# Kernel tuning notes

Measured on AMD Instinct MI355X. Metric: run time of the kernel, lower is better.

## Reference

```python
import jax, jax.numpy as jnp
import numpy as np

IMG = 32            # feature-map side == image_size
B, HC = 8, 3        # batch, hint channels
C, NH, L = 256, 8, 8  # model_channels, nhead, num_encoder_layers
DFF = 1025
HIN = IMG * 8       # hint resolution (three stride-2 convs => /8)
NEIGH = (7, 7)
CONV_SHAPES = [(16, HC), (16, 16), (32, 16), (32, 32), (96, 32), (96, 96), (256, 96), (C, 256)]
STRIDES = [1, 1, 2, 1, 2, 1, 2, 1]


def setup_inputs() -> dict:
    key = jax.random.key(0)
    ks = jax.random.split(key, 32)
    inp = {"hint": jax.random.normal(ks[0], (B, HC, HIN, HIN), jnp.float32)}
    for i, (co, ci) in enumerate(CONV_SHAPES):
        inp[f"conv_w{i}"] = jax.random.normal(ks[1 + i], (co, ci, 3, 3), jnp.float32) * 0.05
    base = 9
    def p(shape, j):
        return jax.random.normal(ks[base + j], (L,) + shape, jnp.float32) * 0.02
    inp["in_proj_w"] = p((3 * C, C), 0)
    inp["in_proj_b"] = p((3 * C,), 1)
    inp["out_w"] = p((C, C), 2)
    inp["out_b"] = p((C,), 3)
    inp["lin1_w"] = p((DFF, C), 4)
    inp["lin1_b"] = p((DFF,), 5)
    inp["lin2_w"] = p((C, DFF), 6)
    inp["lin2_b"] = p((C,), 7)
    inp["ln1_w"] = jnp.ones((L, C), jnp.float32)
    inp["ln1_b"] = jnp.zeros((L, C), jnp.float32)
    inp["ln2_w"] = jnp.ones((L, C), jnp.float32)
    inp["ln2_b"] = jnp.zeros((L, C), jnp.float32)
    return inp


def _conv(x, w, s):
    # torch Conv2d(k=3, padding=1, stride=s, bias=False)
    return jax.lax.conv_general_dilated(x, w, (s, s), [(1, 1), (1, 1)],
                                        dimension_numbers=("NCHW", "OIHW", "NCHW"))


def _sine_pos(h, w, c):
    # DETR/UniAD PositionEmbeddingSine (normalize=False, temperature=1e4) -> (h*w, c)
    npf = c // 2
    y = jnp.broadcast_to(jnp.arange(1, h + 1, dtype=jnp.float32)[:, None], (h, w))
    x = jnp.broadcast_to(jnp.arange(1, w + 1, dtype=jnp.float32)[None, :], (h, w))
    dim_t = 10000.0 ** (2.0 * (jnp.arange(npf, dtype=jnp.float32) // 2) / npf)
    px = x[..., None] / dim_t
    py = y[..., None] / dim_t
    px = jnp.stack([jnp.sin(px[..., 0::2]), jnp.cos(px[..., 1::2])], -1).reshape(h, w, npf)
    py = jnp.stack([jnp.sin(py[..., 0::2]), jnp.cos(py[..., 1::2])], -1).reshape(h, w, npf)
    return jnp.concatenate([py, px], -1).reshape(h * w, c)


def _neigh_mask(h, w, hm, wm):
    # vectorized version of generate_mask: 0 inside the hm x wm neighborhood, -inf outside
    ih = jnp.arange(h)
    iw = jnp.arange(w)
    dh = jnp.abs(ih[:, None] - ih[None, :]) <= hm // 2   # (h, h)
    dw = jnp.abs(iw[:, None] - iw[None, :]) <= wm // 2   # (w, w)
    allowed = (dh[:, None, :, None] & dw[None, :, None, :]).reshape(h * w, h * w)
    return jnp.where(allowed, 0.0, -1e9).astype(jnp.float32)


def _ln(x, g, b):
    mu = x.mean(-1, keepdims=True)
    v = ((x - mu) ** 2).mean(-1, keepdims=True)
    return (x - mu) / jnp.sqrt(v + 1e-5) * g + b


def _forward(hint, conv_ws, params):
    x = hint
    for i, (w, s) in enumerate(zip(conv_ws, STRIDES)):
        x = _conv(x, w, s)
        if i < len(conv_ws) - 1:
            x = jax.nn.silu(x)
    b, c, h, w = x.shape
    src = x.reshape(b, c, h * w).transpose(0, 2, 1)          # (B, N, C), N h-major
    pos = _sine_pos(h, w, c)[None]                           # (1, N, C)
    mask = _neigh_mask(h, w, *NEIGH)                         # (N, N)
    dh = c // NH
    scale = 1.0 / np.sqrt(dh).astype(np.float32)

    def layer(s, p):
        ipw, ipb, ow, ob, l1w, l1b, l2w, l2b, g1, b1, g2, b2 = p
        qk_in = s + pos
        q = (qk_in @ ipw[:c].T + ipb[:c]).reshape(b, -1, NH, dh)
        k = (qk_in @ ipw[c:2 * c].T + ipb[c:2 * c]).reshape(b, -1, NH, dh)
        v = (s @ ipw[2 * c:].T + ipb[2 * c:]).reshape(b, -1, NH, dh)
        sc = jnp.einsum('bnhd,bmhd->bhnm', q, k) * scale + mask
        a = jax.nn.softmax(sc, -1)
        ctx = jnp.einsum('bhnm,bmhd->bnhd', a, v).reshape(b, -1, c)
        s = _ln(s + ctx @ ow.T + ob, g1, b1)                 # post-norm
        ff = jax.nn.relu(s @ l1w.T + l1b) @ l2w.T + l2b      # dropout inactive (eval)
        return _ln(s + ff, g2, b2), None

    src, _ = jax.lax.scan(layer, src, params)
    return src.transpose(0, 2, 1).reshape(b, c, h, w)        # '(h w) b c -> b c h w'


def reference(hint, conv_w0, conv_w1, conv_w2, conv_w3, conv_w4, conv_w5, conv_w6, conv_w7,
              in_proj_w, in_proj_b, out_w, out_b, lin1_w, lin1_b, lin2_w, lin2_b,
              ln1_w, ln1_b, ln2_w, ln2_b):
    conv_ws = (conv_w0, conv_w1, conv_w2, conv_w3, conv_w4, conv_w5, conv_w6, conv_w7)
    params = (in_proj_w, in_proj_b, out_w, out_b, lin1_w, lin1_b, lin2_w, lin2_b,
              ln1_w, ln1_b, ln2_w, ln2_b)
    return _forward(hint, conv_ws, params)
```

## Files before the change

kernel.cpp:

```cpp
#include <hip/hip_runtime.h>
#include <hip/hip_bf16.h>


typedef __bf16 bf16x8 __attribute__((ext_vector_type(8)));
typedef float f32x4 __attribute__((ext_vector_type(4)));
typedef unsigned short us8v __attribute__((ext_vector_type(8)));

__device__ __forceinline__ unsigned short f2bf(float f) {
  unsigned int u = __float_as_uint(f);
  unsigned int r = (u + 0x7fffu + ((u >> 16) & 1u)) >> 16;
  return (unsigned short)r;
}
__device__ __forceinline__ float bf2f(unsigned short h) {
  return __uint_as_float(((unsigned int)h) << 16);
}

#define GLD16(src, dst)                                                        \
  __builtin_amdgcn_global_load_lds(                                            \
      (const __attribute__((address_space(1))) unsigned int*)(src),            \
      (__attribute__((address_space(3))) unsigned int*)(dst), 16, 0, 0)

template<int BM, int BN, int NT, int MODE, int LNF = 0, int KTC = 0>
__global__ __launch_bounds__(NT) void k_gemm(
    const unsigned short* __restrict__ A, int lda,
    const unsigned short* __restrict__ Bw, int ldb,
    const float* __restrict__ bias, const float* __restrict__ posadd,
    float* __restrict__ C, unsigned short* __restrict__ Cb, int ldc,
    int K, int Nstore, int act, int omode, long long zsB, long long zsC,
    const unsigned short* __restrict__ zpage, int Ci, int Hi, int stride, int lw,
    int divm, int divs, const float* __restrict__ lng, const float* __restrict__ lnb)
{
  constexpr int NW = NT / 64;
  constexpr int NWN = (NT == 512) ? 4 : ((BN >= 128) ? 2 : 1);
  constexpr int NWM = NW / NWN;
  constexpr int WM = BM / NWM, WN = BN / NWN;
  constexpr int MF = WM / 16, NF = WN / 16;
  constexpr int AIS = (BM * 8) / NT;
  constexpr int BIS = (BN * 8) / NT;
  __shared__ unsigned short lA[2][BM * 64];
  __shared__ unsigned short lB[2][BN * 64];
  __shared__ float red[2][32][2];
  int tid = threadIdx.x, lane = tid & 63, wid = tid >> 6;
  int bm = blockIdx.x * BM, bn = blockIdx.y * BN;
  const unsigned short* Bz = Bw + (size_t)blockIdx.z * zsB;

  int j = (lane & 7) ^ (lane >> 3);
  int e8 = (j & 3) << 3;
  int halfl = j >> 2;

  size_t arow[AIS], brow[BIS];
  int hb[AIS], wb[AIS];
  size_t ab[AIS];
#pragma unroll
  for (int i = 0; i < AIS; ++i) {
    int rr = (wid + i * NW) * 8 + (lane >> 3);
    if constexpr (MODE == 0) {
      arow[i] = (size_t)(bm + rr) * lda + (j << 3);
    } else {
      int pos = bm + rr;
      int b = pos >> (2 * lw);
      int rem = pos & ((1 << (2 * lw)) - 1);
      int ho = rem >> lw, wo = rem & ((1 << lw) - 1);
      hb[i] = ho * stride - 1;
      wb[i] = wo * stride - 1;
      ab[i] = (size_t)b * Hi * Hi * Ci;
    }
  }
#pragma unroll
  for (int i = 0; i < BIS; ++i)
    brow[i] = (size_t)(bn + (wid + i * NW) * 8 + (lane >> 3)) * ldb + (j << 3);

  auto stage = [&](int buf, int kt) {
    if constexpr (MODE == 1) {
      int s0 = kt * 2, s1 = s0 + 1;
      int t0 = (s0 * divm) >> divs, t1 = (s1 * divm) >> divs;
      int cipw = Ci >> 5;
      int cc0 = (s0 - t0 * cipw) << 5, cc1 = (s1 - t1 * cipw) << 5;
      int kh0 = (t0 * 171) >> 9, kw0 = t0 - kh0 * 3;
      int kh1 = (t1 * 171) >> 9, kw1 = t1 - kh1 * 3;
      int kh = halfl ? kh1 : kh0;
      int kw = halfl ? kw1 : kw0;
      int cco = halfl ? cc1 : cc0;
      bool tv = (halfl ? t1 : t0) < 9;
#pragma unroll
      for (int i = 0; i < AIS; ++i) {
        int hi = hb[i] + kh, wi = wb[i] + kw;
        const unsigned short* ap =
            (tv && (unsigned)hi < (unsigned)Hi && (unsigned)wi < (unsigned)Hi)
                ? (A + ab[i] + (size_t)(hi * Hi + wi) * Ci + cco + e8)
                : zpage;
        GLD16(ap, &lA[buf][(wid + i * NW) * 512]);
      }
    } else {
#pragma unroll
      for (int i = 0; i < AIS; ++i)
        GLD16(A + arow[i] + kt * 64, &lA[buf][(wid + i * NW) * 512]);
    }
#pragma unroll
    for (int i = 0; i < BIS; ++i)
      GLD16(Bz + brow[i] + kt * 64, &lB[buf][(wid + i * NW) * 512]);
  };

  f32x4 acc[MF][NF];
#pragma unroll
  for (int m = 0; m < MF; ++m)
#pragma unroll
    for (int n = 0; n < NF; ++n)
#pragma unroll
      for (int q = 0; q < 4; ++q) acc[m][n][q] = 0.f;

  int wn = wid % NWN, wm = wid / NWN;
  int r0 = wm * WM + (lane & 15);
  int c0 = wn * WN + (lane & 15);
  int sl0 = (((lane >> 4)) ^ (lane & 7)) << 3;
  int sl1 = (((lane >> 4) + 4) ^ (lane & 7)) << 3;
  const int nkt = (KTC > 0) ? KTC : (K >> 6);
  int cur = 0;
  stage(0, 0);
#pragma unroll
  for (int kt = 0; kt < nkt; ++kt) {
    if (kt + 1 < nkt) {
      stage(cur ^ 1, kt + 1);
      asm volatile("s_waitcnt vmcnt(%0)" : : "n"(AIS + BIS) : "memory");
    } else {
      asm volatile("s_waitcnt vmcnt(0)" : : : "memory");
    }
    __builtin_amdgcn_s_barrier();
    asm volatile("" ::: "memory");
    bf16x8 a0[MF], a1[MF], b0[NF], b1[NF];
#pragma unroll
    for (int m = 0; m < MF; ++m) {
      a0[m] = *(const bf16x8*)&lA[cur][(r0 + m * 16) * 64 + sl0];
      a1[m] = *(const bf16x8*)&lA[cur][(r0 + m * 16) * 64 + sl1];
    }
#pragma unroll
    for (int n = 0; n < NF; ++n) {
      b0[n] = *(const bf16x8*)&lB[cur][(c0 + n * 16) * 64 + sl0];
      b1[n] = *(const bf16x8*)&lB[cur][(c0 + n * 16) * 64 + sl1];
    }
#pragma unroll
    for (int m = 0; m < MF; ++m)
#pragma unroll
      for (int n = 0; n < NF; ++n)
        acc[m][n] = __builtin_amdgcn_mfma_f32_16x16x32_bf16(a0[m], b0[n], acc[m][n], 0, 0, 0);
#pragma unroll
    for (int m = 0; m < MF; ++m)
#pragma unroll
      for (int n = 0; n < NF; ++n)
        acc[m][n] = __builtin_amdgcn_mfma_f32_16x16x32_bf16(a1[m], b1[n], acc[m][n], 0, 0, 0);
    asm volatile("" ::: "memory");
    __builtin_amdgcn_s_barrier();
    cur ^= 1;
  }

  int colb = bn + wn * WN + (lane & 15);
  int rowb = bm + wm * WM + ((lane >> 4) << 2);

  if constexpr (LNF) {
    float x[NF][4];
    float sums[4] = {0.f, 0.f, 0.f, 0.f}, sqs[4] = {0.f, 0.f, 0.f, 0.f};
#pragma unroll
    for (int n = 0; n < NF; ++n) {
      int col = colb + n * 16;
      float bs = bias[col];
#pragma unroll
      for (int q = 0; q < 4; ++q) {
        int row = rowb + q;
        float v = acc[0][n][q] + bs + C[(size_t)row * 256 + col];
        x[n][q] = v;
        sums[q] += v;
        sqs[q] += v * v;
      }
    }
#pragma unroll
    for (int q = 0; q < 4; ++q) {
      sums[q] += __shfl_xor(sums[q], 1); sqs[q] += __shfl_xor(sqs[q], 1);
      sums[q] += __shfl_xor(sums[q], 2); sqs[q] += __shfl_xor(sqs[q], 2);
      sums[q] += __shfl_xor(sums[q], 4); sqs[q] += __shfl_xor(sqs[q], 4);
      sums[q] += __shfl_xor(sums[q], 8); sqs[q] += __shfl_xor(sqs[q], 8);
    }
    int rl = wm * 16 + ((lane >> 4) << 2);
    if ((lane & 15) == 0) {
#pragma unroll
      for (int q = 0; q < 4; ++q) {
        red[wn][rl + q][0] = sums[q];
        red[wn][rl + q][1] = sqs[q];
      }
    }
    __syncthreads();
#pragma unroll
    for (int q = 0; q < 4; ++q) {
      float ts = sums[q] + red[wn ^ 1][rl + q][0];
      float tq = sqs[q] + red[wn ^ 1][rl + q][1];
      float mu = ts * (1.f / 256.f);
      float var = tq * (1.f / 256.f) - mu * mu;
      float rs = rsqrtf(var + 1e-5f);
      int row = rowb + q;
#pragma unroll
      for (int n = 0; n < NF; ++n) {
        int col = colb + n * 16;
        float o = (x[n][q] - mu) * rs * lng[col] + lnb[col];
        C[(size_t)row * 256 + col] = o;
        Cb[(size_t)row * 256 + col] = f2bf(o);
      }
    }
    return;
  }

  float* Cz = C ? C + (size_t)blockIdx.z * zsC : nullptr;
  unsigned short* Cbz = Cb ? Cb + (size_t)blockIdx.z * zsC : nullptr;
#pragma unroll
  for (int n = 0; n < NF; ++n) {
    int col = colb + n * 16;
    if (col >= Nstore) continue;
    float bs = bias ? bias[col] : 0.f;
#pragma unroll
    for (int m = 0; m < MF; ++m) {
#pragma unroll
      for (int q = 0; q < 4; ++q) {
        int row = rowb + m * 16 + q;
        float v = acc[m][n][q] + bs;
        if (posadd && col < 512) v += posadd[((row & 1023) << 9) + col];
        if (act == 1) v = fmaxf(v, 0.f);
        else if (act == 2) v = v / (1.f + __expf(-v));
        size_t off = (size_t)row * ldc + col;
        if (omode == 0) Cz[off] = v;
        else if (omode == 1) Cbz[off] = f2bf(v);
        else { Cz[off] = v; Cbz[off] = f2bf(v); }
      }
    }
  }
}

__global__ __launch_bounds__(256) void k_conv0(
    const float* __restrict__ x, const float* __restrict__ w,
    unsigned short* __restrict__ y)
{
  __shared__ float ws[16][28];
  int tid = threadIdx.x;
  for (int u = tid; u < 432; u += 256) {
    int co = u / 27, k = u - co * 27;
    int t = k / 3, ci = k - t * 3;
    ws[co][k] = w[((size_t)co * 3 + ci) * 9 + t];
  }
  __syncthreads();
  int h = blockIdx.x, b = blockIdx.y, wo = tid;
  float xin[3][3][3];
#pragma unroll
  for (int ci = 0; ci < 3; ++ci)
#pragma unroll
    for (int kh = 0; kh < 3; ++kh) {
      int hi = h + kh - 1;
#pragma unroll
      for (int kw = 0; kw < 3; ++kw) {
        int wi = wo + kw - 1;
        xin[ci][kh][kw] = ((unsigned)hi < 256u && (unsigned)wi < 256u)
            ? x[(((size_t)b * 3 + ci) << 16) + (hi << 8) + wi] : 0.f;
      }
    }
  float acc[16] = {};
#pragma unroll
  for (int t = 0; t < 9; ++t) {
    const int kh = t / 3, kw = t % 3;
#pragma unroll
    for (int ci = 0; ci < 3; ++ci) {
      float xv = xin[ci][kh][kw];
#pragma unroll
      for (int co = 0; co < 16; ++co)
        acc[co] = fmaf(xv, ws[co][t * 3 + ci], acc[co]);
    }
  }
  us8v o0, o1, zv;
#pragma unroll
  for (int q = 0; q < 8; ++q) {
    float v0 = acc[q];     v0 = v0 / (1.f + __expf(-v0)); o0[q] = f2bf(v0);
    float v1 = acc[q + 8]; v1 = v1 / (1.f + __expf(-v1)); o1[q] = f2bf(v1);
    zv[q] = 0;
  }
  unsigned short* yp = y + ((((size_t)b << 16) + (h << 8) + wo) << 5);
  *(us8v*)(yp) = o0; *(us8v*)(yp + 8) = o1;
  *(us8v*)(yp + 16) = zv; *(us8v*)(yp + 24) = zv;
}

template<int S>
__global__ __launch_bounds__(256) void k_conv_direct(
    const unsigned short* __restrict__ x, const unsigned short* __restrict__ wp,
    int ldw, unsigned short* __restrict__ y, int Hi, int Ho, int Wo, int lwt)
{
  constexpr int HR = 7 * S + 3;
  constexpr int HC = 15 * S + 3;
  constexpr int HP = HR * HC;
  __shared__ unsigned short xs[HP * 40];
  __shared__ unsigned short wsh[32 * 312];
  int tid = threadIdx.x, lane = tid & 63, wv = tid >> 6;
  int b = blockIdx.y;
  int tr = blockIdx.x >> lwt, tc = blockIdx.x & ((1 << lwt) - 1);
  int hi0 = tr * 8 * S - 1, wi0 = tc * 16 * S - 1;

  for (int u = tid; u < HP * 8; u += 256) {
    int pix = u >> 3, part = u & 7;
    int hr = pix / HC, hcc = pix - hr * HC;
    int hi = hi0 + hr, wi = wi0 + hcc;
    ushort4 v = {0, 0, 0, 0};
    if ((unsigned)hi < (unsigned)Hi && (unsigned)wi < (unsigned)Hi)
      v = *(const ushort4*)(x + ((size_t)(b * Hi + hi) * Hi + wi) * 32 + part * 4);
    *(ushort4*)(&xs[pix * 40 + part * 4]) = v;
  }
  for (int u = tid; u < 2304; u += 256) {
    int co = u / 72, kk = (u - co * 72) * 4;
    *(ushort4*)(&wsh[co * 312 + kk]) = *(const ushort4*)(wp + (size_t)co * ldw + kk);
  }
  __syncthreads();

  int cL = lane & 15, kq = (lane >> 4) << 3;
  f32x4 acc[2][2];
#pragma unroll
  for (int m = 0; m < 2; ++m)
#pragma unroll
    for (int n = 0; n < 2; ++n)
#pragma unroll
      for (int q = 0; q < 4; ++q) acc[m][n][q] = 0.f;

#pragma unroll
  for (int tap = 0; tap < 9; ++tap) {
    const int kh = tap / 3, kw = tap % 3;
    bf16x8 af[2], bfr[2];
#pragma unroll
    for (int m = 0; m < 2; ++m) {
      int hr = (wv * 2 + m) * S + kh;
      int hc = cL * S + kw;
      af[m] = *(const bf16x8*)&xs[(hr * HC + hc) * 40 + kq];
    }
#pragma unroll
    for (int n = 0; n < 2; ++n)
      bfr[n] = *(const bf16x8*)&wsh[(cL + n * 16) * 312 + tap * 32 + kq];
#pragma unroll
    for (int m = 0; m < 2; ++m)
#pragma unroll
      for (int n = 0; n < 2; ++n)
        acc[m][n] = __builtin_amdgcn_mfma_f32_16x16x32_bf16(af[m], bfr[n], acc[m][n], 0, 0, 0);
  }

  int wo0 = tc * 16 + ((lane >> 4) << 2);
#pragma unroll
  for (int m = 0; m < 2; ++m) {
    int ho = tr * 8 + wv * 2 + m;
#pragma unroll
    for (int n = 0; n < 2; ++n) {
      int co = cL + n * 16;
#pragma unroll
      for (int q = 0; q < 4; ++q) {
        float v = acc[m][n][q];
        v = v / (1.f + __expf(-v));
        y[((size_t)(b * Ho + ho) * Wo + wo0 + q) * 32 + co] = f2bf(v);
      }
    }
  }
}

struct WP8 { const float* w[8]; unsigned short* q[8]; };
__global__ __launch_bounds__(256) void k_wperm_all(WP8 p)
{
  const int CoPs[8]  = {128, 32, 32, 32, 128, 128, 256, 256};
  const int CiRs[8]  = {3, 16, 16, 32, 32, 96, 96, 256};
  const int CiPs[8]  = {3, 32, 32, 32, 32, 96, 96, 256};
  const int Kpads[8] = {64, 288, 288, 288, 320, 896, 896, 2304};
  const int Cos[8]   = {16, 16, 32, 32, 96, 96, 256, 256};
  int i = blockIdx.y + 1;
  const float* w = p.w[i];
  unsigned short* wp = p.q[i];
  int Kpad = Kpads[i], CiP = CiPs[i], CiR = CiRs[i], Co = Cos[i];
  int total = CoPs[i] * Kpad;
  for (int idx = blockIdx.x * 256 + threadIdx.x; idx < total; idx += gridDim.x * 256) {
    int co = idx / Kpad, k = idx - co * Kpad;
    int t = k / CiP, ci = k - t * CiP;
    float v = 0.f;
    if (co < Co && t < 9 && ci < CiR) v = w[((size_t)co * CiR + ci) * 9 + t];
    wp[idx] = f2bf(v);
  }
}

__global__ void k_cvt_pad(const float* __restrict__ in, unsigned short* __restrict__ outb,
                          float* __restrict__ outf, int R, int C, int Rp, int Cp)
{
  int l = blockIdx.y;
  int total = Rp * Cp;
  for (int idx = blockIdx.x * 256 + threadIdx.x; idx < total; idx += gridDim.x * 256) {
    int r = idx / Cp, c = idx - r * Cp;
    float v = (r < R && c < C) ? in[((size_t)l * R + r) * C + c] : 0.f;
    size_t o = (size_t)l * total + idx;
    if (outb) outb[o] = f2bf(v);
    if (outf) outf[o] = v;
  }
}

__global__ __launch_bounds__(256) void k_pos(unsigned short* __restrict__ posb)
{
  int n = blockIdx.x, c = threadIdx.x;
  int ih = n >> 5, iw = n & 31;
  float coord = (c < 128) ? (float)(ih + 1) : (float)(iw + 1);
  int cc = c & 127;
  float e = (float)((cc >> 1) << 1) * (1.f / 128.f);
  float t = coord / powf(10000.f, e);
  posb[(n << 8) + c] = f2bf((cc & 1) ? cosf(t) : sinf(t));
}

__global__ __launch_bounds__(256) void k_attn(
    const unsigned short* __restrict__ qkv, unsigned short* __restrict__ ctx)
{
  __shared__ unsigned short k_ldsu[848 * 8];
  __shared__ unsigned short v_lds[848 * 8];
  __shared__ float p_lds[64 * 50];
  int bx = blockIdx.x;
  int b = bx >> 4, tile = bx & 15;
  int th8 = ((tile >> 2) << 3), tw8 = ((tile & 3) << 3);
  int g = blockIdx.y;
  int tid = threadIdx.x, lane = tid & 63, wid = tid >> 6;
  int h0e = max(th8 - 3, 0), h1e = min(th8 + 10, 31);
  int w0e = max(tw8 - 3, 0), w1e = min(tw8 + 10, 31);
  int nh = h1e - h0e + 1, nw = w1e - w0e + 1;
  int nkeys = nh * nw, nslots = nkeys * 4;
  unsigned int magic = (65536u + (unsigned)nw - 1u) / (unsigned)nw;
  size_t qbase = (size_t)((unsigned)b << 10) * 768;

#pragma unroll
  for (int i = 0; i < 4; ++i) {
    int base = i * 256 + wid * 64;
    if (base < 784) {
      int s = min(base + lane, nslots - 1);
      int uidx = s >> 2, chunk = s & 3;
      int hh = (int)(((unsigned)uidx * magic) >> 16);
      int ww = uidx - hh * nw;
      hh += h0e; ww += w0e;
      const unsigned short* rp = qkv + qbase + (size_t)((hh << 5) + ww) * 768 + (g << 5) + chunk * 8;
      GLD16(rp + 256, &k_ldsu[base * 8]);
      GLD16(rp + 512, &v_lds[base * 8]);
    }
  }
  __syncthreads();

  int q = tid >> 2, dq = tid & 3;
  int qh = th8 + (q >> 3), qw = tw8 + (q & 7);
  const float scale = 0.17677669529663687f;
  const unsigned short* qp = qkv + qbase + (size_t)((qh << 5) + qw) * 768 + (g << 5) + dq * 8;
  us8v uq = *(const us8v*)qp;
  float qr[8];
#pragma unroll
  for (int t = 0; t < 8; ++t) qr[t] = bf2f(uq[t]) * scale;

  int rbase[7], cofs[7];
  bool rval[7], cval[7];
#pragma unroll
  for (int d = 0; d < 7; ++d) {
    int mh = qh - 3 + d;
    rval[d] = (unsigned)mh < 32u;
    rbase[d] = (mh - h0e) * nw;
    int mw = qw - 3 + d;
    cval[d] = (unsigned)mw < 32u;
    cofs[d] = mw - w0e;
  }

  float m = -1e30f;
#pragma unroll
  for (int kk = 0; kk < 49; ++kk) {
    const int d7 = kk / 7, r7 = kk % 7;
    bool valid = rval[d7] && cval[r7];
    int uidx = valid ? (rbase[d7] + cofs[r7]) : 0;
    us8v uk = *(const us8v*)&k_ldsu[uidx * 32 + dq * 8];
    float d = 0.f;
#pragma unroll
    for (int t = 0; t < 8; ++t) d = fmaf(qr[t], bf2f(uk[t]), d);
    d += __shfl_xor(d, 1);
    d += __shfl_xor(d, 2);
    float s_kk = valid ? d : -1e30f;
    m = fmaxf(m, s_kk);
    if (dq == (kk & 3)) p_lds[q * 50 + kk] = s_kk;
  }
  float sum = 0.f;
  for (int kk = dq; kk < 49; kk += 4) {
    float e = __expf(p_lds[q * 50 + kk] - m);
    p_lds[q * 50 + kk] = e;
    sum += e;
  }
  sum += __shfl_xor(sum, 1);
  sum += __shfl_xor(sum, 2);
  float inv = 1.f / sum;

  float acc[8] = {};
#pragma unroll
  for (int kk = 0; kk < 49; ++kk) {
    const int d7 = kk / 7, r7 = kk % 7;
    int uidx = (rval[d7] && cval[r7]) ? (rbase[d7] + cofs[r7]) : 0;
    float pb = p_lds[q * 50 + kk];
    us8v uv = *(const us8v*)&v_lds[uidx * 32 + dq * 8];
#pragma unroll
    for (int t = 0; t < 8; ++t) acc[t] = fmaf(pb, bf2f(uv[t]), acc[t]);
  }
  unsigned short* op = ctx + ((size_t)((b << 10) + (qh << 5) + qw) << 8) + (g << 5) + dq * 8;
  us8v out;
#pragma unroll
  for (int t = 0; t < 8; ++t) out[t] = f2bf(acc[t] * inv);
  *(us8v*)op = out;
}

__global__ void k_nxc_to_cxn(const float* __restrict__ x, float* __restrict__ y)
{
  __shared__ float t[32][33];
  int b = blockIdx.z;
  int c0 = blockIdx.x * 32, n0 = blockIdx.y * 32;
  int tx = threadIdx.x, ty = threadIdx.y;
  t[ty][tx] = x[((size_t)(b * 1024 + n0 + ty)) * 256 + c0 + tx];
  __syncthreads();
  y[((size_t)(b * 256 + c0 + ty)) * 1024 + n0 + tx] = t[tx][ty];
}

extern "C" void kernel_launch(void* const* d_in, const int* in_sizes, int n_in,
                              void* d_out, int out_size, void* d_ws, size_t ws_size,
                              hipStream_t stream)
{
  const float* hint = (const float*)d_in[0];
  const float* cw[8];
  for (int i = 0; i < 8; ++i) cw[i] = (const float*)d_in[1 + i];
  const float* ipw  = (const float*)d_in[9];
  const float* ipb  = (const float*)d_in[10];
  const float* outw = (const float*)d_in[11];
  const float* outb = (const float*)d_in[12];
  const float* l1w  = (const float*)d_in[13];
  const float* l1b  = (const float*)d_in[14];
  const float* l2w  = (const float*)d_in[15];
  const float* l2b  = (const float*)d_in[16];
  const float* g1   = (const float*)d_in[17];
  const float* b1   = (const float*)d_in[18];
  const float* g2   = (const float*)d_in[19];
  const float* b2   = (const float*)d_in[20];

  float* ws = (float*)d_ws;
  size_t off = 0;
  float* bufA = ws + off; off += 8388608;
  float* bufB = ws + off; off += 8388608;
  float* src  = ws + off; off += 2097152;
  unsigned short* srcb = (unsigned short*)(ws + off); off += 1048576;
  unsigned short* posb = (unsigned short*)(ws + off); off += 131072;
  float* posqk = ws + off; off += 4194304;
  unsigned short* wqkvb = (unsigned short*)(ws + off); off += 786432;
  unsigned short* outwb = (unsigned short*)(ws + off); off += 262144;
  unsigned short* l1wb  = (unsigned short*)(ws + off); off += 1179648;
  unsigned short* l2wb  = (unsigned short*)(ws + off); off += 1179648;
  float* l1bp = ws + off; off += 9216;
  unsigned short* cwp[8];
  const int CoPs[8]  = {128, 32, 32, 32, 128, 128, 256, 256};
  const int Kpads[8] = {64, 288, 288, 288, 320, 896, 896, 2304};
  for (int i = 0; i < 8; ++i) { cwp[i] = (unsigned short*)(ws + off); off += ((size_t)CoPs[i] * Kpads[i] + 1) / 2; }
  unsigned short* zpage = (unsigned short*)(ws + off); off += 64;

  hipMemsetAsync(zpage, 0, 256, stream);

  k_cvt_pad<<<dim3(768, 8), 256, 0, stream>>>(ipw,  wqkvb, nullptr, 768, 256, 768, 256);
  k_cvt_pad<<<dim3(256, 8), 256, 0, stream>>>(outw, outwb, nullptr, 256, 256, 256, 256);
  k_cvt_pad<<<dim3(1152, 8), 256, 0, stream>>>(l1w, l1wb, nullptr, 1025, 256, 1152, 256);
  k_cvt_pad<<<dim3(1152, 8), 256, 0, stream>>>(l2w, l2wb, nullptr, 256, 1025, 256, 1152);
  k_cvt_pad<<<dim3(5, 8), 256, 0, stream>>>(l1b, nullptr, l1bp, 1025, 1, 1152, 1);
  WP8 wpargs;
  for (int i = 0; i < 8; ++i) { wpargs.w[i] = cw[i]; wpargs.q[i] = cwp[i]; }
  k_wperm_all<<<dim3(64, 7), 256, 0, stream>>>(wpargs);
  k_pos<<<dim3(1024), 256, 0, stream>>>(posb);

  unsigned short* bufAu = (unsigned short*)bufA;
  unsigned short* bufBu = (unsigned short*)bufB;

#define GEMM_TAIL nullptr, 0, 0, 0, 0, 0, 0, nullptr, nullptr
  k_conv0<<<dim3(256, 8), 256, 0, stream>>>(hint, cw[0], bufAu);
  k_conv_direct<1><<<dim3(512, 8), 256, 0, stream>>>(bufAu, cwp[1], 288, bufBu, 256, 256, 256, 4);
  k_conv_direct<2><<<dim3(128, 8), 256, 0, stream>>>(bufBu, cwp[2], 288, bufAu, 256, 128, 128, 3);
  k_conv_direct<1><<<dim3(128, 8), 256, 0, stream>>>(bufAu, cwp[3], 288, bufBu, 128, 128, 128, 3);
  k_gemm<128, 128, 512, 1, 0, 5><<<dim3(256, 1), 512, 0, stream>>>(
      bufBu, 0, cwp[4], 320, nullptr, nullptr, nullptr, bufAu, 96, 320, 96, 2, 1,
      0, 0, zpage, 32, 128, 2, 6, 1, 0, nullptr, nullptr);
  k_gemm<128, 128, 512, 1, 0, 14><<<dim3(256, 1), 512, 0, stream>>>(
      bufAu, 0, cwp[5], 896, nullptr, nullptr, nullptr, bufBu, 96, 896, 96, 2, 1,
      0, 0, zpage, 96, 64, 1, 6, 171, 9, nullptr, nullptr);
  k_gemm<64, 128, 512, 1, 0, 14><<<dim3(128, 2), 512, 0, stream>>>(
      bufBu, 0, cwp[6], 896, nullptr, nullptr, nullptr, bufAu, 256, 896, 256, 2, 1,
      0, 0, zpage, 96, 64, 2, 5, 171, 9, nullptr, nullptr);
  k_gemm<64, 128, 512, 1><<<dim3(128, 2), 512, 0, stream>>>(
      bufAu, 0, cwp[7], 2304, nullptr, nullptr, src, srcb, 256, 2304, 256, 0, 2,
      0, 0, zpage, 256, 32, 1, 5, 1, 3, nullptr, nullptr);

  k_gemm<64, 128, 512, 0, 0, 4><<<dim3(16, 4, 8), 512, 0, stream>>>(
      posb, 256, wqkvb, 256, nullptr, nullptr, posqk, nullptr, 512, 256, 512, 0, 0,
      196608LL, 524288LL, GEMM_TAIL);

  unsigned short* qkvb = bufAu;
  unsigned short* ctx  = (unsigned short*)(bufA + 3145728);
  unsigned short* ff   = (unsigned short*)(bufB + 2097152);

  for (int l = 0; l < 8; ++l) {
    const unsigned short* wqkv_l = wqkvb + (size_t)l * 768 * 256;
    const float* ipb_l  = ipb  + (size_t)l * 768;
    const unsigned short* outw_l = outwb + (size_t)l * 256 * 256;
    const float* outb_l = outb + (size_t)l * 256;
    const unsigned short* l1w_l = l1wb + (size_t)l * 1152 * 256;
    const float* l1b_l  = l1bp + (size_t)l * 1152;
    const unsigned short* l2w_l = l2wb + (size_t)l * 256 * 1152;
    const float* l2b_l  = l2b  + (size_t)l * 256;
    const float* posqk_l = posqk + (size_t)l * 524288;
    const float* g1_l = g1 + l * 256; const float* b1_l = b1 + l * 256;
    const float* g2_l = g2 + l * 256; const float* b2_l = b2 + l * 256;

    k_gemm<64, 128, 512, 0, 0, 4><<<dim3(128, 6), 512, 0, stream>>>(
        srcb, 256, wqkv_l, 256, ipb_l, posqk_l, nullptr, qkvb, 768, 256, 768, 0, 1,
        0, 0, GEMM_TAIL);
    k_attn<<<dim3(128, 8), 256, 0, stream>>>(qkvb, ctx);
    k_gemm<32, 256, 256, 0, 1, 4><<<dim3(256, 1), 256, 0, stream>>>(
        ctx, 256, outw_l, 256, outb_l, nullptr, src, srcb, 256, 256, 256, 0, 0,
        0, 0, nullptr, 0, 0, 0, 0, 0, 0, g1_l, b1_l);
    k_gemm<64, 128, 512, 0, 0, 4><<<dim3(128, 9), 512, 0, stream>>>(
        srcb, 256, l1w_l, 256, l1b_l, nullptr, nullptr, ff, 1152, 256, 1152, 1, 1,
        0, 0, GEMM_TAIL);
    k_gemm<32, 256, 256, 0, 1, 18><<<dim3(256, 1), 256, 0, stream>>>(
        ff, 1152, l2w_l, 1152, l2b_l, nullptr, src, srcb, 256, 1152, 256, 0, 0,
        0, 0, nullptr, 0, 0, 0, 0, 0, 0, g2_l, b2_l);
  }

  k_nxc_to_cxn<<<dim3(8, 32, 8), dim3(32, 32), 0, stream>>>(src, (float*)d_out);
}
```

Baseline: 911.9 us.

## Fuse FFN lin1+ReLU+lin2+LayerNorm into one kernel; merge prep launches

Adds a fused FFN kernel in which each 32-row block computes the lin1 GEMM with bias and ReLU into a 32x1152 bf16 LDS tile, then runs the lin2 GEMM, residual add and LayerNorm without writing the intermediate to global memory. It uses double-buffered global-to-LDS weight staging. This removes one launch per layer and the global round-trip of the 8192x1152 intermediate. The trade-off is 256 blocks with very large LDS use (about 140KB), so occupancy is low and the weights are re-read by every block. Separately, the weight-conversion and positional-embedding setup kernels are merged into one launch.

```diff
diff --git a/kernel.cpp b/kernel.cpp
--- a/kernel.cpp
+++ b/kernel.cpp
@@ -232,6 +232,191 @@
   }
 }
 
+__global__ __launch_bounds__(256) void k_ffn(
+    const unsigned short* __restrict__ srcb, const unsigned short* __restrict__ w1,
+    const float* __restrict__ b1, const unsigned short* __restrict__ w2,
+    const float* __restrict__ b2, float* __restrict__ src,
+    unsigned short* __restrict__ sbo,
+    const float* __restrict__ lng, const float* __restrict__ lnb)
+{
+  __shared__ unsigned short aT[4][32 * 64];
+  __shared__ unsigned short lB[2][256 * 64];
+  __shared__ unsigned short ffl[32][1160];
+  __shared__ float red[2][32][2];
+  int tid = threadIdx.x, lane = tid & 63, wid = tid >> 6;
+  int bm = blockIdx.x << 5;
+  int j = (lane & 7) ^ (lane >> 3);
+  int rsrc = (lane >> 3);
+
+  {
+    int rr = wid * 8 + rsrc;
+    const unsigned short* ap = srcb + (size_t)(bm + rr) * 256 + (j << 3);
+#pragma unroll
+    for (int kt = 0; kt < 4; ++kt)
+      GLD16(ap + kt * 64, &aT[kt][wid * 512]);
+  }
+  size_t brow1[4], brow2[8];
+#pragma unroll
+  for (int i = 0; i < 4; ++i)
+    brow1[i] = (size_t)((wid + i * 4) * 8 + rsrc) * 256 + (j << 3);
+#pragma unroll
+  for (int i = 0; i < 8; ++i)
+    brow2[i] = (size_t)((wid + i * 4) * 8 + rsrc) * 1152 + (j << 3);
+
+  auto stageB1 = [&](int buf, int s) {
+    int ny = s >> 2, kt = s & 3;
+#pragma unroll
+    for (int i = 0; i < 4; ++i)
+      GLD16(w1 + (size_t)ny * 128 * 256 + brow1[i] + kt * 64, &lB[buf][(wid + i * 4) * 512]);
+  };
+  auto stageB2 = [&](int buf, int kt) {
+#pragma unroll
+    for (int i = 0; i < 8; ++i)
+      GLD16(w2 + brow2[i] + kt * 64, &lB[buf][(wid + i * 4) * 512]);
+  };
+
+  int wn = wid & 1, wm = wid >> 1;
+  int r0 = wm * 16 + (lane & 15);
+  int sl0 = (((lane >> 4)) ^ (lane & 7)) << 3;
+  int sl1 = (((lane >> 4) + 4) ^ (lane & 7)) << 3;
+  int kqa = (lane >> 4) << 3;
+
+  stageB1(0, 0);
+  int cur = 0;
+  for (int ny = 0; ny < 9; ++ny) {
+    f32x4 acc1[4];
+#pragma unroll
+    for (int n = 0; n < 4; ++n)
+#pragma unroll
+      for (int q = 0; q < 4; ++q) acc1[n][q] = 0.f;
+    int c01 = wn * 64 + (lane & 15);
+#pragma unroll
+    for (int kt = 0; kt < 4; ++kt) {
+      int s = ny * 4 + kt;
+      if (s + 1 < 36) {
+        stageB1(cur ^ 1, s + 1);
+        asm volatile("s_waitcnt vmcnt(4)" : : : "memory");
+      } else {
+        asm volatile("s_waitcnt vmcnt(0)" : : : "memory");
+      }
+      __builtin_amdgcn_s_barrier();
+      asm volatile("" ::: "memory");
+      bf16x8 a0 = *(const bf16x8*)&aT[kt][r0 * 64 + sl0];
+      bf16x8 a1 = *(const bf16x8*)&aT[kt][r0 * 64 + sl1];
+      bf16x8 b0v[4], b1v[4];
+#pragma unroll
+      for (int n = 0; n < 4; ++n) {
+        b0v[n] = *(const bf16x8*)&lB[cur][(c01 + n * 16) * 64 + sl0];
+        b1v[n] = *(const bf16x8*)&lB[cur][(c01 + n * 16) * 64 + sl1];
+      }
+#pragma unroll
+      for (int n = 0; n < 4; ++n)
+        acc1[n] = __builtin_amdgcn_mfma_f32_16x16x32_bf16(a0, b0v[n], acc1[n], 0, 0, 0);
+#pragma unroll
+      for (int n = 0; n < 4; ++n)
+        acc1[n] = __builtin_amdgcn_mfma_f32_16x16x32_bf16(a1, b1v[n], acc1[n], 0, 0, 0);
+      asm volatile("" ::: "memory");
+      __builtin_amdgcn_s_barrier();
+      cur ^= 1;
+    }
+    int rowl = wm * 16 + ((lane >> 4) << 2);
+#pragma unroll
+    for (int n = 0; n < 4; ++n) {
+      int col = ny * 128 + c01 + n * 16;
+      float bs = b1[col];
+#pragma unroll
+      for (int q = 0; q < 4; ++q)
+        ffl[rowl + q][col] = f2bf(fmaxf(acc1[n][q] + bs, 0.f));
+    }
+  }
+
+  stageB2(0, 0);
+  __syncthreads();
+  cur = 0;
+  f32x4 acc[8];
+#pragma unroll
+  for (int n = 0; n < 8; ++n)
+#pragma unroll
+    for (int q = 0; q < 4; ++q) acc[n][q] = 0.f;
+  int c02 = wn * 128 + (lane & 15);
+#pragma unroll
+  for (int kt = 0; kt < 18; ++kt) {
+    if (kt + 1 < 18) {
+      stageB2(cur ^ 1, kt + 1);
+      asm volatile("s_waitcnt vmcnt(8)" : : : "memory");
+    } else {
+      asm volatile("s_waitcnt vmcnt(0)" : : : "memory");
+    }
+    __builtin_amdgcn_s_barrier();
+    asm volatile("" ::: "memory");
+    bf16x8 a0 = *(const bf16x8*)&ffl[r0][kt * 64 + kqa];
+    bf16x8 a1 = *(const bf16x8*)&ffl[r0][kt * 64 + 32 + kqa];
+    bf16x8 b0v[8], b1v[8];
+#pragma unroll
+    for (int n = 0; n < 8; ++n) {
+      b0v[n] = *(const bf16x8*)&lB[cur][(c02 + n * 16) * 64 + sl0];
+      b1v[n] = *(const bf16x8*)&lB[cur][(c02 + n * 16) * 64 + sl1];
+    }
+#pragma unroll
+    for (int n = 0; n < 8; ++n)
+      acc[n] = __builtin_amdgcn_mfma_f32_16x16x32_bf16(a0, b0v[n], acc[n], 0, 0, 0);
+#pragma unroll
+    for (int n = 0; n < 8; ++n)
+      acc[n] = __builtin_amdgcn_mfma_f32_16x16x32_bf16(a1, b1v[n], acc[n], 0, 0, 0);
+    asm volatile("" ::: "memory");
+    __builtin_amdgcn_s_barrier();
+    cur ^= 1;
+  }
+
+  int rowl = wm * 16 + ((lane >> 4) << 2);
+  float x[8][4];
+  float sums[4] = {0.f, 0.f, 0.f, 0.f}, sqs[4] = {0.f, 0.f, 0.f, 0.f};
+#pragma unroll
+  for (int n = 0; n < 8; ++n) {
+    int col = c02 + n * 16;
+    float bs = b2[col];
+#pragma unroll
+    for (int q = 0; q < 4; ++q) {
+      int row = bm + rowl + q;
+      float v = acc[n][q] + bs + src[(size_t)row * 256 + col];
+      x[n][q] = v;
+      sums[q] += v;
+      sqs[q] += v * v;
+    }
+  }
+#pragma unroll
+  for (int q = 0; q < 4; ++q) {
+    sums[q] += __shfl_xor(sums[q], 1); sqs[q] += __shfl_xor(sqs[q], 1);
+    sums[q] += __shfl_xor(sums[q], 2); sqs[q] += __shfl_xor(sqs[q], 2);
+    sums[q] += __shfl_xor(sums[q], 4); sqs[q] += __shfl_xor(sqs[q], 4);
+    sums[q] += __shfl_xor(sums[q], 8); sqs[q] += __shfl_xor(sqs[q], 8);
+  }
+  if ((lane & 15) == 0) {
+#pragma unroll
+    for (int q = 0; q < 4; ++q) {
+      red[wn][rowl + q][0] = sums[q];
+      red[wn][rowl + q][1] = sqs[q];
+    }
+  }
+  __syncthreads();
+#pragma unroll
+  for (int q = 0; q < 4; ++q) {
+    float ts = sums[q] + red[wn ^ 1][rowl + q][0];
+    float tq = sqs[q] + red[wn ^ 1][rowl + q][1];
+    float mu = ts * (1.f / 256.f);
+    float var = tq * (1.f / 256.f) - mu * mu;
+    float rs = rsqrtf(var + 1e-5f);
+    int row = bm + rowl + q;
+#pragma unroll
+    for (int n = 0; n < 8; ++n) {
+      int col = c02 + n * 16;
+      float o = (x[n][q] - mu) * rs * lng[col] + lnb[col];
+      src[(size_t)row * 256 + col] = o;
+      sbo[(size_t)row * 256 + col] = f2bf(o);
+    }
+  }
+}
+
 __global__ __launch_bounds__(256) void k_conv0(
     const float* __restrict__ x, const float* __restrict__ w,
     unsigned short* __restrict__ y)
@@ -380,29 +565,48 @@
   }
 }
 
-__global__ void k_cvt_pad(const float* __restrict__ in, unsigned short* __restrict__ outb,
-                          float* __restrict__ outf, int R, int C, int Rp, int Cp)
+struct PrepArgs {
+  const float *ipw, *outw, *l1w, *l2w, *l1b;
+  unsigned short *wqkvb, *outwb, *l1wb, *l2wb, *posb;
+  float *l1bp;
+};
+__global__ __launch_bounds__(256) void k_prep(PrepArgs a)
 {
-  int l = blockIdx.y;
-  int total = Rp * Cp;
-  for (int idx = blockIdx.x * 256 + threadIdx.x; idx < total; idx += gridDim.x * 256) {
-    int r = idx / Cp, c = idx - r * Cp;
-    float v = (r < R && c < C) ? in[((size_t)l * R + r) * C + c] : 0.f;
-    size_t o = (size_t)l * total + idx;
-    if (outb) outb[o] = f2bf(v);
-    if (outf) outf[o] = v;
-  }
-}
-
-__global__ __launch_bounds__(256) void k_pos(unsigned short* __restrict__ posb)
-{
-  int n = blockIdx.x, c = threadIdx.x;
-  int ih = n >> 5, iw = n & 31;
-  float coord = (c < 128) ? (float)(ih + 1) : (float)(iw + 1);
-  int cc = c & 127;
-  float e = (float)((cc >> 1) << 1) * (1.f / 128.f);
-  float t = coord / powf(10000.f, e);
-  posb[(n << 8) + c] = f2bf((cc & 1) ? cosf(t) : sinf(t));
+  int seg = blockIdx.y;
+  int idx0 = blockIdx.x * 256 + threadIdx.x;
+  int stride = gridDim.x * 256;
+  if (seg == 0) {
+    for (int i = idx0; i < 8 * 768 * 256; i += stride) a.wqkvb[i] = f2bf(a.ipw[i]);
+  } else if (seg == 1) {
+    for (int i = idx0; i < 8 * 256 * 256; i += stride) a.outwb[i] = f2bf(a.outw[i]);
+  } else if (seg == 2) {
+    for (int i = idx0; i < 8 * 1152 * 256; i += stride) {
+      int l = i / (1152 * 256), r = (i >> 8) % 1152, c = i & 255;
+      float v = (r < 1025) ? a.l1w[((size_t)l * 1025 + r) * 256 + c] : 0.f;
+      a.l1wb[i] = f2bf(v);
+    }
+  } else if (seg == 3) {
+    for (int i = idx0; i < 8 * 256 * 1152; i += stride) {
+      int l = i / (256 * 1152), rc = i % (256 * 1152), r = rc / 1152, c = rc - (rc / 1152) * 1152;
+      float v = (c < 1025) ? a.l2w[((size_t)l * 256 + r) * 1025 + c] : 0.f;
+      a.l2wb[i] = f2bf(v);
+    }
+  } else if (seg == 4) {
+    for (int i = idx0; i < 8 * 1152; i += stride) {
+      int l = i / 1152, c = i - l * 1152;
+      a.l1bp[i] = (c < 1025) ? a.l1b[l * 1025 + c] : 0.f;
+    }
+  } else {
+    for (int i = idx0; i < 1024 * 256; i += stride) {
+      int n = i >> 8, c = i & 255;
+      int ih = n >> 5, iw = n & 31;
+      float coord = (c < 128) ? (float)(ih + 1) : (float)(iw + 1);
+      int cc = c & 127;
+      float e = (float)((cc >> 1) << 1) * (1.f / 128.f);
+      float t = coord / powf(10000.f, e);
+      a.posb[i] = f2bf((cc & 1) ? cosf(t) : sinf(t));
+    }
+  }
 }
 
 __global__ __launch_bounds__(256) void k_attn(
@@ -555,15 +759,14 @@
 
   hipMemsetAsync(zpage, 0, 256, stream);
 
-  k_cvt_pad<<<dim3(768, 8), 256, 0, stream>>>(ipw,  wqkvb, nullptr, 768, 256, 768, 256);
-  k_cvt_pad<<<dim3(256, 8), 256, 0, stream>>>(outw, outwb, nullptr, 256, 256, 256, 256);
-  k_cvt_pad<<<dim3(1152, 8), 256, 0, stream>>>(l1w, l1wb, nullptr, 1025, 256, 1152, 256);
-  k_cvt_pad<<<dim3(1152, 8), 256, 0, stream>>>(l2w, l2wb, nullptr, 256, 1025, 256, 1152);
-  k_cvt_pad<<<dim3(5, 8), 256, 0, stream>>>(l1b, nullptr, l1bp, 1025, 1, 1152, 1);
+  PrepArgs pa;
+  pa.ipw = ipw; pa.outw = outw; pa.l1w = l1w; pa.l2w = l2w; pa.l1b = l1b;
+  pa.wqkvb = wqkvb; pa.outwb = outwb; pa.l1wb = l1wb; pa.l2wb = l2wb;
+  pa.posb = posb; pa.l1bp = l1bp;
+  k_prep<<<dim3(256, 6), 256, 0, stream>>>(pa);
   WP8 wpargs;
   for (int i = 0; i < 8; ++i) { wpargs.w[i] = cw[i]; wpargs.q[i] = cwp[i]; }
   k_wperm_all<<<dim3(64, 7), 256, 0, stream>>>(wpargs);
-  k_pos<<<dim3(1024), 256, 0, stream>>>(posb);
 
   unsigned short* bufAu = (unsigned short*)bufA;
   unsigned short* bufBu = (unsigned short*)bufB;
@@ -592,7 +795,6 @@
 
   unsigned short* qkvb = bufAu;
   unsigned short* ctx  = (unsigned short*)(bufA + 3145728);
-  unsigned short* ff   = (unsigned short*)(bufB + 2097152);
 
   for (int l = 0; l < 8; ++l) {
     const unsigned short* wqkv_l = wqkvb + (size_t)l * 768 * 256;
@@ -614,12 +816,8 @@
     k_gemm<32, 256, 256, 0, 1, 4><<<dim3(256, 1), 256, 0, stream>>>(
         ctx, 256, outw_l, 256, outb_l, nullptr, src, srcb, 256, 256, 256, 0, 0,
         0, 0, nullptr, 0, 0, 0, 0, 0, 0, g1_l, b1_l);
-    k_gemm<64, 128, 512, 0, 0, 4><<<dim3(128, 9), 512, 0, stream>>>(
-        srcb, 256, l1w_l, 256, l1b_l, nullptr, nullptr, ff, 1152, 256, 1152, 1, 1,
-        0, 0, GEMM_TAIL);
-    k_gemm<32, 256, 256, 0, 1, 18><<<dim3(256, 1), 256, 0, stream>>>(
-        ff, 1152, l2w_l, 1152, l2b_l, nullptr, src, srcb, 256, 1152, 256, 0, 0,
-        0, 0, nullptr, 0, 0, 0, 0, 0, 0, g2_l, b2_l);
+    k_ffn<<<dim3(256), 256, 0, stream>>>(
+        srcb, l1w_l, l1b_l, l2w_l, l2b_l, src, srcb, g2_l, b2_l);
   }
 
   k_nxc_to_cxn<<<dim3(8, 32, 8), dim3(32, 32), 0, stream>>>(src, (float*)d_out);
```

Result: faster. 887.0 us (-2.7%).
